# Optimization experiments

Measured on AMD Instinct MI355X. Metric: run time of the kernel, lower is better.

## Reference

```python
import jax, jax.numpy as jnp
import numpy as np

N = 100000   # nodes per layer
E = 600000   # edges per block
FIN = 256    # raw feature dim
H = 128      # hidden_size
C = 47       # n_classes
L = 3        # num_layers = n_layers + 1
NOUT = 10000 # seed nodes
GEN_EPS = 1e-7
T = 1.0
LN_EPS = 1e-5


def setup_inputs() -> dict:
    key = jax.random.key(0)
    ks = jax.random.split(key, 10)
    return {
        "x": jax.random.normal(ks[0], (N, FIN), jnp.float32),
        "src": jax.random.randint(ks[1], (L - 1, E), 0, N),
        "dst": jax.random.randint(ks[2], (L - 1, E), 0, N),
        "node_map": jax.random.randint(ks[3], (L - 1, N), 0, N),
        "final_map": jax.random.randint(ks[4], (NOUT,), 0, N),
        "enc_w": jax.random.normal(ks[5], (FIN, H), jnp.float32) * 0.05,
        "enc_b": jnp.zeros((H,), jnp.float32),
        "gcn_w": jax.random.normal(ks[6], (L, H, H), jnp.float32) * 0.05,
        "gcn_b": jnp.zeros((L, H), jnp.float32),
        "ln_g": jnp.ones((L, H), jnp.float32),
        "ln_b": jnp.zeros((L, H), jnp.float32),
        "pred_w": jax.random.normal(ks[7], (H, C), jnp.float32) * 0.05,
        "pred_b": jnp.zeros((C,), jnp.float32),
    }


def _layer_norm(h, g, b):
    mu = jnp.mean(h, axis=-1, keepdims=True)
    var = jnp.mean(jnp.square(h - mu), axis=-1, keepdims=True)
    return (h - mu) * jax.lax.rsqrt(var + LN_EPS) * g + b


def _gen_conv(h, src, dst, w, b):
    # GENConv, aggr='softmax', mlp_layers=1, no edge_attr, no msg_norm.
    m = jax.nn.relu(h[src]) + GEN_EPS                      # [E, H] messages
    # per-destination, per-feature segment softmax with temperature T
    mx = jax.ops.segment_max(m * T, dst, num_segments=N)   # [N, H]
    e = jnp.exp(m * T - mx[dst])                           # [E, H]
    denom = jax.ops.segment_sum(e, dst, num_segments=N)    # [N, H]
    alpha = e / (denom[dst] + 1e-16)
    agg = jax.ops.segment_sum(m * alpha, dst, num_segments=N)  # [N, H]
    return (agg + h) @ w + b                               # residual + Linear (MLP)


def reference(x, src, dst, node_map, final_map, enc_w, enc_b,
              gcn_w, gcn_b, ln_g, ln_b, pred_w, pred_b):
    h = x @ enc_w + enc_b                                  # node_features_encoder
    h = _gen_conv(h, src[0], dst[0], gcn_w[0], gcn_b[0])   # gcns[0] with block-0 edges
    for layer in range(1, L):                              # res+ block
        h2 = jax.nn.relu(_layer_norm(h, ln_g[layer - 1], ln_b[layer - 1]))
        # dropout is identity in eval mode (p applied with training=False)
        # gcns[layer] uses the edge_index set BEFORE this iteration's move
        h = _gen_conv(h2, src[layer - 1], dst[layer - 1],
                      gcn_w[layer], gcn_b[layer]) + h
        h = h[node_map[layer - 1]]                         # nf_move_layer_to gather
    h = jax.nn.relu(_layer_norm(h, ln_g[L - 1], ln_b[L - 1]))
    h = h @ pred_w + pred_b                                # node_pred_linear
    h = h[final_map]                                       # seed-node extraction
    return jax.nn.log_softmax(h, axis=-1)
```

## Files before the change

kernel.cpp:

```cpp
#include <hip/hip_runtime.h>
#include <hip/hip_bf16.h>
#include <hip/hip_fp16.h>

typedef unsigned short u16;
typedef unsigned int u32;

#define N_NODES 100000
#define N_EDGES 600000
#define FIN_D   256
#define HDIM    128
#define NCLS    47
#define NOUT_D  10000
#define NCHUNK  196
#define NP2     100352
#define PCH     2048
#define PNB     ((N_EDGES + PCH - 1) / PCH)

typedef short bf16x8 __attribute__((ext_vector_type(8)));
typedef float f32x4  __attribute__((ext_vector_type(4)));

#define GPTR(p) (const __attribute__((address_space(1))) u32*)(p)
#define LPTR(p) (__attribute__((address_space(3))) u32*)(p)

__device__ __forceinline__ float bf2f(u16 u) {
    union { u32 i; float f; } v; v.i = ((u32)u) << 16; return v.f;
}
__device__ __forceinline__ u16 f2bf(float f) {
    __hip_bfloat16 h = __float2bfloat16(f);
    return *reinterpret_cast<u16*>(&h);
}
__device__ __forceinline__ float loadF(const void* p, size_t i, bool f32) {
    if (f32) return ((const float*)p)[i];
    return bf2f(((const u16*)p)[i]);
}
__device__ __forceinline__ float wave_sum(float v) {
    #pragma unroll
    for (int o = 32; o > 0; o >>= 1) v += __shfl_xor(v, o, 64);
    return v;
}
__device__ __forceinline__ float wave_max(float v) {
    #pragma unroll
    for (int o = 32; o > 0; o >>= 1) v = fmaxf(v, __shfl_xor(v, o, 64));
    return v;
}
__device__ __forceinline__ int wave_sum_i(int v) {
    #pragma unroll
    for (int o = 32; o > 0; o >>= 1) v += __shfl_xor(v, o, 64);
    return v;
}
__device__ __forceinline__ int block_excl_scan_256(int v, int* wsum) {
    int lane = threadIdx.x & 63, wv = threadIdx.x >> 6;
    int inc = v;
    #pragma unroll
    for (int off = 1; off < 64; off <<= 1) {
        int u = __shfl_up(inc, off, 64);
        if (lane >= off) inc += u;
    }
    if (lane == 63) wsum[wv] = inc;
    __syncthreads();
    if (threadIdx.x == 0) {
        int a = 0;
        #pragma unroll
        for (int w = 0; w < 4; ++w) { int t = wsum[w]; wsum[w] = a; a += t; }
    }
    __syncthreads();
    return inc - v + wsum[wv];
}

__global__ __launch_bounds__(256) void dtype_detect_kernel(
    const u16* __restrict__ x, int* __restrict__ flag)
{
    int i = blockIdx.x * 256 + threadIdx.x;
    u32 e = (x[i] >> 7) & 0xFF;
    unsigned long long b = __ballot(e >= 200);
    if ((threadIdx.x & 63) == 0) {
        int c = __popcll(b);
        if (c) atomicAdd(&flag[1], c);
    }
}

__global__ __launch_bounds__(256) void hist2_kernel(
    const int* __restrict__ dst, int* __restrict__ deg2, int egrid)
{
    int half = (blockIdx.x >= egrid) ? 1 : 0;
    int e = (blockIdx.x - half * egrid) * 256 + threadIdx.x;
    if (e < N_EDGES) atomicAdd(&deg2[half * NP2 + dst[half * N_EDGES + e]], 1);
}

__global__ __launch_bounds__(256) void csum2_kernel(
    const int* __restrict__ deg2, int* __restrict__ csum)
{
    __shared__ int ws[4];
    int half = (blockIdx.x >= NCHUNK) ? 1 : 0;
    int b = blockIdx.x - half * NCHUNK;
    int i0 = half * NP2 + b * 512 + threadIdx.x;
    int v = 0;
    if (b * 512 + threadIdx.x < N_NODES) v += deg2[i0];
    if (b * 512 + threadIdx.x + 256 < N_NODES) v += deg2[i0 + 256];
    v = wave_sum_i(v);
    int lane = threadIdx.x & 63, wv = threadIdx.x >> 6;
    if (lane == 0) ws[wv] = v;
    __syncthreads();
    if (threadIdx.x == 0)
        csum[blockIdx.x] = ws[0] + ws[1] + ws[2] + ws[3];
}

__global__ __launch_bounds__(256) void coff2_kernel(
    const int* __restrict__ csum, int* __restrict__ coff,
    int* __restrict__ bcur)
{
    __shared__ int wsum[4];
    int t = threadIdx.x;
    for (int h = 0; h < 2; ++h) {
        int v = (t < NCHUNK) ? csum[h * NCHUNK + t] : 0;
        int excl = block_excl_scan_256(v, wsum);
        if (t < NCHUNK) {
            coff[h * NCHUNK + t] = excl;
            bcur[(h * NCHUNK + t) * 16] = excl;
        }
        __syncthreads();
    }
}

__global__ __launch_bounds__(256) void scan2_kernel(
    const int* __restrict__ deg2, const int* __restrict__ coff,
    int* __restrict__ rp0, int* __restrict__ rp1)
{
    __shared__ int wsum[4];
    int half = (blockIdx.x >= NCHUNK) ? 1 : 0;
    int b = blockIdx.x - half * NCHUNK;
    const int* deg = deg2 + half * NP2;
    int* rp = half ? rp1 : rp0;
    int t = threadIdx.x;
    int i0 = b * 512 + 2 * t;
    int d0 = (i0 < N_NODES) ? deg[i0] : 0;
    int d1 = (i0 + 1 < N_NODES) ? deg[i0 + 1] : 0;
    int excl = block_excl_scan_256(d0 + d1, wsum);
    int base = coff[half * NCHUNK + b] + excl;
    if (i0 < N_NODES)     rp[i0] = base;
    if (i0 + 1 < N_NODES) rp[i0 + 1] = base + d0;
    if (b == 0 && t == 0) rp[N_NODES] = N_EDGES;
}

__global__ __launch_bounds__(256) void bucket_part_kernel(
    const int* __restrict__ src, const int* __restrict__ dst,
    const int* __restrict__ comp1,
    int* __restrict__ bcur, int2* __restrict__ tmp)
{
    __shared__ int hist[NCHUNK];
    __shared__ int base[NCHUNK];
    int half = (blockIdx.x >= PNB) ? 1 : 0;
    int b = blockIdx.x - half * PNB;
    int e0 = b * PCH;
    for (int i = threadIdx.x; i < NCHUNK; i += 256) hist[i] = 0;
    __syncthreads();

    int2 loc[8];
    #pragma unroll
    for (int t = 0; t < 8; ++t) {
        int e = e0 + t * 256 + threadIdx.x;
        loc[t].y = -1;
        if (e < N_EDGES) {
            int ge = half * N_EDGES + e;
            int d = dst[ge];
            int s = src[ge];
            if (half) s = comp1[s];
            loc[t] = make_int2(s, d);
            atomicAdd(&hist[d >> 9], 1);
        }
    }
    __syncthreads();
    for (int i = threadIdx.x; i < NCHUNK; i += 256) {
        int h = hist[i];
        base[i] = (h > 0) ? atomicAdd(&bcur[(half * NCHUNK + i) * 16], h) : 0;
        hist[i] = 0;
    }
    __syncthreads();
    #pragma unroll
    for (int t = 0; t < 8; ++t) {
        if (loc[t].y >= 0) {
            int bk = loc[t].y >> 9;
            int pos = base[bk] + atomicAdd(&hist[bk], 1);
            tmp[(size_t)half * N_EDGES + pos] = loc[t];
        }
    }
}

__global__ __launch_bounds__(256) void bucket_sort_kernel(
    const int2* __restrict__ tmp,
    const int* __restrict__ rp0, const int* __restrict__ rp1,
    const int* __restrict__ coff, const int* __restrict__ csum,
    int* __restrict__ ei0, int* __restrict__ ei1)
{
    __shared__ int cur[512];
    int half = (blockIdx.x >= NCHUNK) ? 1 : 0;
    int b = blockIdx.x - half * NCHUNK;
    const int* rp = half ? rp1 : rp0;
    int* ei = half ? ei1 : ei0;
    int n0 = b * 512;
    #pragma unroll
    for (int i = threadIdx.x; i < 512; i += 256) {
        int n = n0 + i;
        cur[i] = (n < N_NODES) ? rp[n] : 0;
    }
    __syncthreads();
    int beg = coff[half * NCHUNK + b];
    int end = beg + csum[half * NCHUNK + b];
    for (int i = beg + threadIdx.x; i < end; i += 256) {
        int2 p = tmp[(size_t)half * N_EDGES + i];
        int pos = atomicAdd(&cur[p.y & 511], 1);
        ei[pos] = p.x;
    }
}

__global__ __launch_bounds__(256) void pack_b_kernel(
    const void* __restrict__ enc_w, const void* __restrict__ gcn_w,
    const int* __restrict__ dt, u16* __restrict__ Bp)
{
    const bool f32 = (dt[1] > 16);
    int o = blockIdx.x * 256 + threadIdx.x;
    if (o >= 32768 + 3 * 16384) return;
    const void* srcp; size_t soff; int m;
    if (o < 32768) { srcp = enc_w; soff = 0; m = o; }
    else {
        int l = (o - 32768) >> 14;
        srcp = gcn_w; soff = (size_t)l * 16384; m = (o - 32768) & 16383;
    }
    int j    = m & 7;
    int lane = (m >> 3) & 63;
    int ct   = (m >> 9) & 7;
    int kidx = m >> 12;
    int k = kidx * 32 + (lane >> 4) * 8 + j;
    int n = ct * 16 + (lane & 15);
    Bp[o] = f2bf(loadF(srcp, soff + (size_t)k * HDIM + n, f32));
}

__global__ __launch_bounds__(256, 2) void enc_gemm_kernel(
    const void* __restrict__ Araw, const u16* __restrict__ Bp,
    const void* __restrict__ bias, const int* __restrict__ dt,
    int rowbase, u16* __restrict__ OutBF)
{
    extern __shared__ char SH[];
    const bool f32 = (dt[1] > 16);
    const int tid  = threadIdx.x;
    const int w    = tid >> 6;
    const int lane = tid & 63;
    const int quad = lane >> 4;
    const int cl   = lane & 15;
    const int m0   = rowbase + blockIdx.x * 16;

    #pragma unroll
    for (int i = 0; i < 16; ++i) {
        int off = (w * 16 + i) * 1024;
        __builtin_amdgcn_global_load_lds(
            GPTR((const char*)Bp + off + lane * 16),
            LPTR(SH + off), 16, 0, 0);
    }
    if (f32) {
        #pragma unroll
        for (int i = 0; i < 4; ++i) {
            int row = w * 4 + i;
            int src = (lane * 16) ^ ((row & 7) << 4);
            __builtin_amdgcn_global_load_lds(
                GPTR((const char*)Araw + (size_t)(m0 + row) * 1024 + src),
                LPTR(SH + 65536 + row * 1024), 16, 0, 0);
        }
    } else {
        #pragma unroll
        for (int i = 0; i < 2; ++i) {
            int r0 = (w * 2 + i) * 2;
            int row = r0 + (lane >> 5);
            int src = ((lane & 31) * 16) ^ ((row & 7) << 4);
            __builtin_amdgcn_global_load_lds(
                GPTR((const char*)Araw + (size_t)(m0 + row) * 512 + src),
                LPTR(SH + 65536 + r0 * 512), 16, 0, 0);
        }
    }

    f32x4 acc[2];
    acc[0] = (f32x4){0.f, 0.f, 0.f, 0.f};
    acc[1] = (f32x4){0.f, 0.f, 0.f, 0.f};
    const int ct0 = w * 2;
    const int swz = (cl & 7) << 4;

    __syncthreads();

    #pragma unroll
    for (int k = 0; k < 8; ++k) {
        bf16x8 av;
        if (f32) {
            const char* rb = SH + 65536 + cl * 1024;
            int lo = (k * 128 + quad * 32) ^ swz;
            float4 v0 = *(const float4*)(rb + lo);
            float4 v1 = *(const float4*)(rb + (lo ^ 16));
            union { u32 u[4]; bf16x8 v; } cv;
            cv.u[0] = (u32)f2bf(v0.x) | ((u32)f2bf(v0.y) << 16);
            cv.u[1] = (u32)f2bf(v0.z) | ((u32)f2bf(v0.w) << 16);
            cv.u[2] = (u32)f2bf(v1.x) | ((u32)f2bf(v1.y) << 16);
            cv.u[3] = (u32)f2bf(v1.z) | ((u32)f2bf(v1.w) << 16);
            av = cv.v;
        } else {
            const char* rb = SH + 65536 + cl * 512;
            av = *(const bf16x8*)(rb + ((k * 64 + quad * 16) ^ swz));
        }
        #pragma unroll
        for (int c = 0; c < 2; ++c) {
            bf16x8 b = *(const bf16x8*)(SH + k * 8192 + (ct0 + c) * 1024 + lane * 16);
            acc[c] = __builtin_amdgcn_mfma_f32_16x16x32_bf16(av, b, acc[c], 0, 0, 0);
        }
    }

    #pragma unroll
    for (int reg = 0; reg < 4; ++reg) {
        int grow = m0 + quad * 4 + reg;
        #pragma unroll
        for (int c = 0; c < 2; ++c) {
            int col = (ct0 + c) * 16 + cl;
            float v = acc[c][reg] + loadF(bias, col, f32);
            OutBF[(size_t)grow * HDIM + col] = f2bf(v);
        }
    }
}

template<bool OWN_MAP>
__global__ __launch_bounds__(256) void agg_msg_kernel(
    const int* __restrict__ rp, const int* __restrict__ eidx,
    const u16* __restrict__ HBin, const int* __restrict__ own_map,
    u16* __restrict__ Amsg)
{
    __shared__ u32 RS[4][16][64];
    int wave = threadIdx.x >> 6;
    int lane = threadIdx.x & 63;
    int n = blockIdx.x * 4 + wave;
    if (n >= N_NODES) return;
    const u32* HB32 = (const u32*)HBin;
    int nn = OWN_MAP ? own_map[n] : n;
    u32 own = HB32[(size_t)nn * 64 + lane];
    int beg = rp[n], end = rp[n + 1];
    float den0 = 0.f, den1 = 0.f, num0 = 0.f, num1 = 0.f;
    for (int c = beg; c < end; c += 16) {
        int cnt = end - c; if (cnt > 16) cnt = 16;
        int e = c + (lane & 15); if (e > end - 1) e = end - 1;
        int ei = eidx[e];
        int nI = (cnt + 3) >> 2;
        #pragma unroll
        for (int i = 0; i < 4; ++i) {
            if (i < nI) {
                int s = __shfl(ei, i * 4 + (lane >> 4), 64);
                __builtin_amdgcn_global_load_lds(
                    GPTR((const char*)HBin + (size_t)s * 256 + (lane & 15) * 16),
                    LPTR(&RS[wave][i * 4][0]), 16, 0, 0);
            }
        }
        asm volatile("s_waitcnt vmcnt(0)" ::: "memory");
        __builtin_amdgcn_sched_barrier(0);
        #pragma unroll
        for (int t = 0; t < 16; ++t) {
            if (t >= cnt) break;
            u32 h = RS[wave][t][lane];
            float m0 = fmaxf(bf2f((u16)(h & 0xffff)), 0.f) + 1e-7f;
            float m1 = fmaxf(bf2f((u16)(h >> 16)),    0.f) + 1e-7f;
            float e0 = __expf(m0), e1 = __expf(m1);
            den0 += e0; num0 += m0 * e0;
            den1 += e1; num1 += m1 * e1;
        }
        asm volatile("s_waitcnt lgkmcnt(0)" ::: "memory");
        __builtin_amdgcn_sched_barrier(0);
    }
    float a0 = num0 / (den0 + 1e-16f) + bf2f((u16)(own & 0xffff));
    float a1 = num1 / (den1 + 1e-16f) + bf2f((u16)(own >> 16));
    ((u32*)Amsg)[(size_t)n * 64 + lane] = (u32)f2bf(a0) | ((u32)f2bf(a1) << 16);
}

template<bool RES, bool OWN_MAP, bool WRITE_LN>
__global__ __launch_bounds__(256) void conv_gemm_kernel(
    const u16* __restrict__ Amsg, const int* __restrict__ own_map,
    const u16* __restrict__ Bp, int Bpbase,
    const void* __restrict__ bias, int biasoff,
    const __half* __restrict__ Resid,
    const void* __restrict__ lng, const void* __restrict__ lnb, int lnoff,
    const int* __restrict__ dt,
    __half* __restrict__ OutH, u16* __restrict__ HBout)
{
    const bool f32 = (dt[1] > 16);
    __shared__ u16 Bsh[16384];
    __shared__ u16 Ash[8192];
    const int tid  = threadIdx.x;
    const int w    = tid >> 6;
    const int lane = tid & 63;
    const int quad = lane >> 4;
    const int cl   = lane & 15;
    const int m0   = blockIdx.x * 64;

    {
        const char* Bp2 = (const char*)(Bp + Bpbase);
        #pragma unroll
        for (int i = 0; i < 8; ++i)
            __builtin_amdgcn_global_load_lds(
                GPTR(Bp2 + i * 4096 + w * 1024 + lane * 16),
                LPTR((char*)Bsh + i * 4096 + w * 1024), 16, 0, 0);
        const char* Ab = (const char*)Amsg + (size_t)m0 * 256;
        #pragma unroll
        for (int i = 0; i < 4; ++i) {
            int row_local = i * 16 + w * 4 + (lane >> 4);
            int off = ((lane & 15) * 16) ^ ((row_local & 7) << 4);
            __builtin_amdgcn_global_load_lds(
                GPTR(Ab + (size_t)row_local * 256 + off),
                LPTR((char*)Ash + i * 4096 + w * 1024), 16, 0, 0);
        }
    }

    __syncthreads();

    const int row_local = w * 16 + cl;
    const char* ar = (const char*)Ash + row_local * 256;
    const int akey = (row_local & 7) << 4;
    bf16x8 afr[4];
    #pragma unroll
    for (int kidx = 0; kidx < 4; ++kidx)
        afr[kidx] = *(const bf16x8*)(ar + ((kidx * 64 + quad * 16) ^ akey));

    f32x4 acc[8];
    #pragma unroll
    for (int ct = 0; ct < 8; ++ct) acc[ct] = (f32x4){0.f, 0.f, 0.f, 0.f};
    #pragma unroll
    for (int kidx = 0; kidx < 4; ++kidx) {
        const u16* bb = Bsh + ((size_t)(kidx * 8) * 64 + lane) * 8;
        #pragma unroll
        for (int ct = 0; ct < 8; ++ct) {
            bf16x8 b = *(const bf16x8*)(bb + (size_t)ct * 512);
            acc[ct] = __builtin_amdgcn_mfma_f32_16x16x32_bf16(afr[kidx], b, acc[ct], 0, 0, 0);
        }
    }

    #pragma unroll
    for (int reg = 0; reg < 4; ++reg) {
        int n = m0 + w * 16 + quad * 4 + reg;
        if (n >= N_NODES) continue;
        size_t rrow = 0;
        if (RES) rrow = (size_t)(OWN_MAP ? own_map[n] : n) * HDIM;
        float v[8];
        float s1 = 0.f, s2 = 0.f;
        #pragma unroll
        for (int ct = 0; ct < 8; ++ct) {
            int col = ct * 16 + cl;
            float x = acc[ct][reg] + loadF(bias, biasoff + col, f32);
            if (RES) x += __half2float(Resid[rrow + col]);
            v[ct] = x;
            OutH[(size_t)n * HDIM + col] = __float2half(x);
            s1 += x; s2 += x * x;
        }
        if (WRITE_LN) {
            #pragma unroll
            for (int o = 1; o < 16; o <<= 1) {
                s1 += __shfl_xor(s1, o, 64);
                s2 += __shfl_xor(s2, o, 64);
            }
            float mu = s1 * (1.0f / 128.0f);
            float var = s2 * (1.0f / 128.0f) - mu * mu;
            float rs = rsqrtf(fmaxf(var, 0.f) + 1e-5f);
            #pragma unroll
            for (int ct = 0; ct < 8; ++ct) {
                int col = ct * 16 + cl;
                float y = fmaxf((v[ct] - mu) * rs * loadF(lng, lnoff + col, f32)
                                + loadF(lnb, lnoff + col, f32), 0.f);
                HBout[(size_t)n * HDIM + col] = f2bf(y);
            }
        }
    }
}

__global__ __launch_bounds__(256) void final_head_kernel(
    const __half* __restrict__ Hsrc, const int* __restrict__ map1,
    const int* __restrict__ fmap,
    const void* __restrict__ g, const void* __restrict__ b, int goff,
    const void* __restrict__ pw, const void* __restrict__ pb,
    const int* __restrict__ dt, void* __restrict__ out)
{
    const bool f32 = (dt[1] > 16);
    __shared__ float pwl[HDIM * 48];
    __shared__ float pbl[64];
    __shared__ float sh[4][HDIM];
    const int tid = threadIdx.x, wave = tid >> 6, lane = tid & 63;

    for (int i = tid; i < HDIM * NCLS; i += 256)
        pwl[(i / NCLS) * 48 + (i % NCLS)] = loadF(pw, i, f32);
    if (tid < NCLS) pbl[tid] = loadF(pb, tid, f32);
    __syncthreads();

    int i = blockIdx.x * 4 + wave;
    int jj = map1[fmap[i]];
    __half2 hv = *((const __half2*)(Hsrc + (size_t)jj * HDIM) + lane);
    float2 v = __half22float2(hv);
    float mu = wave_sum(v.x + v.y) * (1.0f / 128.0f);
    float d0 = v.x - mu, d1 = v.y - mu;
    float var = wave_sum(d0 * d0 + d1 * d1) * (1.0f / 128.0f);
    float rs = rsqrtf(var + 1e-5f);
    int f0 = lane * 2;
    sh[wave][f0]     = fmaxf(d0 * rs * loadF(g, goff + f0, f32)     + loadF(b, goff + f0, f32),     0.0f);
    sh[wave][f0 + 1] = fmaxf(d1 * rs * loadF(g, goff + f0 + 1, f32) + loadF(b, goff + f0 + 1, f32), 0.0f);
    float acc = -1e30f;
    if (lane < NCLS) {
        acc = pbl[lane];
        #pragma unroll 8
        for (int k = 0; k < HDIM; ++k)
            acc = fmaf(sh[wave][k], pwl[k * 48 + lane], acc);
    }
    float mx = wave_max(acc);
    float ex = (lane < NCLS) ? __expf(acc - mx) : 0.0f;
    float sum = wave_sum(ex);
    if (lane < NCLS) {
        float r = acc - mx - logf(sum);
        if (f32) ((float*)out)[(size_t)i * NCLS + lane] = r;
        else     ((u16*)out)[(size_t)i * NCLS + lane] = f2bf(r);
    }
}

extern "C" void kernel_launch(void* const* d_in, const int* in_sizes, int n_in,
                              void* d_out, int out_size, void* d_ws, size_t ws_size,
                              hipStream_t stream) {
    const void* x       = d_in[0];
    const int* src      = (const int*)d_in[1];
    const int* dst      = (const int*)d_in[2];
    const int* node_map = (const int*)d_in[3];
    const int* fmap     = (const int*)d_in[4];
    const void* enc_w   = d_in[5];
    const void* enc_b   = d_in[6];
    const void* gcn_w   = d_in[7];
    const void* gcn_b   = d_in[8];
    const void* ln_g    = d_in[9];
    const void* ln_b    = d_in[10];
    const void* pred_w  = d_in[11];
    const void* pred_b  = d_in[12];

    char* ws = (char*)d_ws;
    const size_t szH = (size_t)N_NODES * HDIM * sizeof(u16);
    __half* Pa  = (__half*)ws;  ws += szH;
    __half* Pb  = (__half*)ws;  ws += szH;
    u16*   HBa  = (u16*)ws;     ws += szH;
    u16*   HBb  = (u16*)ws;     ws += szH;
    u16*   Amsg = (u16*)ws;     ws += szH;
    int*   FLAG = (int*)ws;     ws += 1024;
    u16*   Bp   = (u16*)ws;     ws += (size_t)(32768 + 3 * 16384) * 2 + 1024;
    int*  deg2  = (int*)ws;  ws += (size_t)2 * NP2 * 4;
    int*  rp0   = (int*)ws;  ws += (size_t)(N_NODES + 2) * 4;
    int*  rp1   = (int*)ws;  ws += (size_t)(N_NODES + 2) * 4;
    int*  ei0   = (int*)ws;  ws += (size_t)N_EDGES * 4;
    int*  ei1   = (int*)ws;  ws += (size_t)N_EDGES * 4;
    int2* tmp   = (int2*)ws; ws += (size_t)2 * N_EDGES * 8;
    int*  csum  = (int*)ws;  ws += 2048;
    int*  coff  = (int*)ws;  ws += 2048;
    int*  bcur  = (int*)ws;  ws += (size_t)2 * NCHUNK * 16 * 4 + 1024;

    dim3 blk(256);
    const int ggrid = (N_NODES + 63) / 64;
    const int gHALF = 3125;
    const int egrid = (N_EDGES + 255) / 256;
    const int agrid = (N_NODES + 3) / 4;
    const int pgrid = (32768 + 3 * 16384 + 255) / 256;

    hipMemsetAsync(FLAG, 0, 64, stream);
    dtype_detect_kernel<<<256, blk, 0, stream>>>((const u16*)x, FLAG);
    pack_b_kernel<<<pgrid, blk, 0, stream>>>(enc_w, gcn_w, FLAG, Bp);

    hipMemsetAsync(deg2, 0, (size_t)2 * NP2 * 4, stream);
    hist2_kernel<<<2 * egrid, blk, 0, stream>>>(dst, deg2, egrid);
    csum2_kernel<<<2 * NCHUNK, blk, 0, stream>>>(deg2, csum);
    coff2_kernel<<<1, blk, 0, stream>>>(csum, coff, bcur);
    scan2_kernel<<<2 * NCHUNK, blk, 0, stream>>>(deg2, coff, rp0, rp1);
    bucket_part_kernel<<<2 * PNB, blk, 0, stream>>>(src, dst, node_map, bcur, tmp);
    bucket_sort_kernel<<<2 * NCHUNK, blk, 0, stream>>>(tmp, rp0, rp1, coff, csum,
                                                       ei0, ei1);

    enc_gemm_kernel<<<gHALF, blk, 81920, stream>>>(x, Bp, enc_b, FLAG, 0, HBa);
    enc_gemm_kernel<<<gHALF, blk, 81920, stream>>>(x, Bp, enc_b, FLAG, 50000, HBa);

    agg_msg_kernel<false><<<agrid, blk, 0, stream>>>(rp0, ei0, HBa, nullptr, Amsg);
    conv_gemm_kernel<false, false, true><<<ggrid, blk, 0, stream>>>(
        Amsg, nullptr, Bp, 32768, gcn_b, 0, nullptr,
        ln_g, ln_b, 0, FLAG, Pa, HBb);

    agg_msg_kernel<false><<<agrid, blk, 0, stream>>>(rp0, ei0, HBb, nullptr, Amsg);
    conv_gemm_kernel<true, false, true><<<ggrid, blk, 0, stream>>>(
        Amsg, nullptr, Bp, 32768 + 16384, gcn_b, 128, Pa,
        ln_g, ln_b, 128, FLAG, Pb, HBa);

    agg_msg_kernel<true><<<agrid, blk, 0, stream>>>(rp1, ei1, HBa, node_map, Amsg);
    conv_gemm_kernel<true, true, false><<<ggrid, blk, 0, stream>>>(
        Amsg, node_map, Bp, 32768 + 2 * 16384, gcn_b, 256, Pb,
        ln_g, ln_b, 256, FLAG, Pa, nullptr);

    final_head_kernel<<<NOUT_D / 4, blk, 0, stream>>>(
        Pa, node_map + N_NODES, fmap, ln_g, ln_b, 256, pred_w, pred_b, FLAG,
        (void*)d_out);
}
```

Before: 574.0 us.

## Fuse softmax aggregation into conv GEMM kernel and merge encoder launches

The per-node softmax aggregation kernel is folded into the conv GEMM kernel. Each 512-thread block has 8 waves that each aggregate 8 destination rows directly into the swizzled shared-memory A tile, then 4 waves run the MFMA GEMM. This drops the Amsg round trip through global memory and halves the kernel launches per layer. The two encoder GEMM launches are also merged into one. The cost is that half the waves sit idle during the GEMM, aggregation batches shrink from 16 to 8 edges, and occupancy may be limited by the larger shared-memory footprint.

```diff
diff --git a/kernel.cpp b/kernel.cpp
--- a/kernel.cpp
+++ b/kernel.cpp
@@ -238,7 +238,7 @@
 __global__ __launch_bounds__(256, 2) void enc_gemm_kernel(
     const void* __restrict__ Araw, const u16* __restrict__ Bp,
     const void* __restrict__ bias, const int* __restrict__ dt,
-    int rowbase, u16* __restrict__ OutBF)
+    u16* __restrict__ OutBF)
 {
     extern __shared__ char SH[];
     const bool f32 = (dt[1] > 16);
@@ -247,7 +247,7 @@
     const int lane = tid & 63;
     const int quad = lane >> 4;
     const int cl   = lane & 15;
-    const int m0   = rowbase + blockIdx.x * 16;
+    const int m0   = blockIdx.x * 16;
 
     #pragma unroll
     for (int i = 0; i < 16; ++i) {
@@ -322,59 +322,10 @@
     }
 }
 
-template<bool OWN_MAP>
-__global__ __launch_bounds__(256) void agg_msg_kernel(
+template<bool RES, bool OWN_MAP, bool WRITE_LN>
+__global__ __launch_bounds__(512, 2) void layer_kernel(
     const int* __restrict__ rp, const int* __restrict__ eidx,
     const u16* __restrict__ HBin, const int* __restrict__ own_map,
-    u16* __restrict__ Amsg)
-{
-    __shared__ u32 RS[4][16][64];
-    int wave = threadIdx.x >> 6;
-    int lane = threadIdx.x & 63;
-    int n = blockIdx.x * 4 + wave;
-    if (n >= N_NODES) return;
-    const u32* HB32 = (const u32*)HBin;
-    int nn = OWN_MAP ? own_map[n] : n;
-    u32 own = HB32[(size_t)nn * 64 + lane];
-    int beg = rp[n], end = rp[n + 1];
-    float den0 = 0.f, den1 = 0.f, num0 = 0.f, num1 = 0.f;
-    for (int c = beg; c < end; c += 16) {
-        int cnt = end - c; if (cnt > 16) cnt = 16;
-        int e = c + (lane & 15); if (e > end - 1) e = end - 1;
-        int ei = eidx[e];
-        int nI = (cnt + 3) >> 2;
-        #pragma unroll
-        for (int i = 0; i < 4; ++i) {
-            if (i < nI) {
-                int s = __shfl(ei, i * 4 + (lane >> 4), 64);
-                __builtin_amdgcn_global_load_lds(
-                    GPTR((const char*)HBin + (size_t)s * 256 + (lane & 15) * 16),
-                    LPTR(&RS[wave][i * 4][0]), 16, 0, 0);
-            }
-        }
-        asm volatile("s_waitcnt vmcnt(0)" ::: "memory");
-        __builtin_amdgcn_sched_barrier(0);
-        #pragma unroll
-        for (int t = 0; t < 16; ++t) {
-            if (t >= cnt) break;
-            u32 h = RS[wave][t][lane];
-            float m0 = fmaxf(bf2f((u16)(h & 0xffff)), 0.f) + 1e-7f;
-            float m1 = fmaxf(bf2f((u16)(h >> 16)),    0.f) + 1e-7f;
-            float e0 = __expf(m0), e1 = __expf(m1);
-            den0 += e0; num0 += m0 * e0;
-            den1 += e1; num1 += m1 * e1;
-        }
-        asm volatile("s_waitcnt lgkmcnt(0)" ::: "memory");
-        __builtin_amdgcn_sched_barrier(0);
-    }
-    float a0 = num0 / (den0 + 1e-16f) + bf2f((u16)(own & 0xffff));
-    float a1 = num1 / (den1 + 1e-16f) + bf2f((u16)(own >> 16));
-    ((u32*)Amsg)[(size_t)n * 64 + lane] = (u32)f2bf(a0) | ((u32)f2bf(a1) << 16);
-}
-
-template<bool RES, bool OWN_MAP, bool WRITE_LN>
-__global__ __launch_bounds__(256) void conv_gemm_kernel(
-    const u16* __restrict__ Amsg, const int* __restrict__ own_map,
     const u16* __restrict__ Bp, int Bpbase,
     const void* __restrict__ bias, int biasoff,
     const __half* __restrict__ Resid,
@@ -385,8 +336,9 @@
     const bool f32 = (dt[1] > 16);
     __shared__ u16 Bsh[16384];
     __shared__ u16 Ash[8192];
+    __shared__ u32 RS[8][8][64];
     const int tid  = threadIdx.x;
-    const int w    = tid >> 6;
+    const int wv   = tid >> 6;
     const int lane = tid & 63;
     const int quad = lane >> 4;
     const int cl   = lane & 15;
@@ -395,22 +347,72 @@
     {
         const char* Bp2 = (const char*)(Bp + Bpbase);
         #pragma unroll
-        for (int i = 0; i < 8; ++i)
+        for (int i = 0; i < 4; ++i)
             __builtin_amdgcn_global_load_lds(
-                GPTR(Bp2 + i * 4096 + w * 1024 + lane * 16),
-                LPTR((char*)Bsh + i * 4096 + w * 1024), 16, 0, 0);
-        const char* Ab = (const char*)Amsg + (size_t)m0 * 256;
-        #pragma unroll
-        for (int i = 0; i < 4; ++i) {
-            int row_local = i * 16 + w * 4 + (lane >> 4);
-            int off = ((lane & 15) * 16) ^ ((row_local & 7) << 4);
-            __builtin_amdgcn_global_load_lds(
-                GPTR(Ab + (size_t)row_local * 256 + off),
-                LPTR((char*)Ash + i * 4096 + w * 1024), 16, 0, 0);
-        }
-    }
-
-    __syncthreads();
+                GPTR(Bp2 + (wv * 4 + i) * 1024 + lane * 16),
+                LPTR((char*)Bsh + (wv * 4 + i) * 1024), 16, 0, 0);
+    }
+
+    const u32* HB32 = (const u32*)HBin;
+    char* AshB = (char*)Ash;
+
+    int rbase = m0 + wv * 8;
+    int ridx = rbase + ((lane < 9) ? lane : 8);
+    if (ridx > N_NODES) ridx = N_NODES;
+    int rpv = rp[ridx];
+
+    #pragma unroll 1
+    for (int j = 0; j < 8; ++j) {
+        int rl = wv * 8 + j;
+        int n = m0 + rl;
+        u32 outv = 0;
+        if (n < N_NODES) {
+            int nn = OWN_MAP ? own_map[n] : n;
+            u32 own = HB32[(size_t)nn * 64 + lane];
+            int beg = __shfl(rpv, j, 64);
+            int end = __shfl(rpv, j + 1, 64);
+            float den0 = 0.f, den1 = 0.f, num0 = 0.f, num1 = 0.f;
+            for (int c = beg; c < end; c += 8) {
+                int cnt = end - c; if (cnt > 8) cnt = 8;
+                int e = c + (lane & 7); if (e > end - 1) e = end - 1;
+                int ei = eidx[e];
+                int nI = (cnt + 3) >> 2;
+                #pragma unroll
+                for (int i = 0; i < 2; ++i) {
+                    if (i < nI) {
+                        int s = __shfl(ei, i * 4 + (lane >> 4), 64);
+                        __builtin_amdgcn_global_load_lds(
+                            GPTR((const char*)HBin + (size_t)s * 256 + (lane & 15) * 16),
+                            LPTR(&RS[wv][i * 4][0]), 16, 0, 0);
+                    }
+                }
+                asm volatile("s_waitcnt vmcnt(0)" ::: "memory");
+                __builtin_amdgcn_sched_barrier(0);
+                #pragma unroll
+                for (int t = 0; t < 8; ++t) {
+                    if (t >= cnt) break;
+                    u32 h = RS[wv][t][lane];
+                    float v0 = fmaxf(bf2f((u16)(h & 0xffff)), 0.f) + 1e-7f;
+                    float v1 = fmaxf(bf2f((u16)(h >> 16)),    0.f) + 1e-7f;
+                    float e0 = __expf(v0), e1 = __expf(v1);
+                    den0 += e0; num0 += v0 * e0;
+                    den1 += e1; num1 += v1 * e1;
+                }
+                asm volatile("s_waitcnt lgkmcnt(0)" ::: "memory");
+                __builtin_amdgcn_sched_barrier(0);
+            }
+            float a0 = num0 / (den0 + 1e-16f) + bf2f((u16)(own & 0xffff));
+            float a1 = num1 / (den1 + 1e-16f) + bf2f((u16)(own >> 16));
+            outv = (u32)f2bf(a0) | ((u32)f2bf(a1) << 16);
+        }
+        *(u32*)(AshB + rl * 256 + ((lane * 4) ^ ((rl & 7) << 4))) = outv;
+    }
+
+    asm volatile("s_waitcnt vmcnt(0)" ::: "memory");
+    __syncthreads();
+
+    if (wv >= 4) return;
+    const int w = wv;
 
     const int row_local = w * 16 + cl;
     const char* ar = (const char*)Ash + row_local * 256;
@@ -539,7 +541,6 @@
     __half* Pb  = (__half*)ws;  ws += szH;
     u16*   HBa  = (u16*)ws;     ws += szH;
     u16*   HBb  = (u16*)ws;     ws += szH;
-    u16*   Amsg = (u16*)ws;     ws += szH;
     int*   FLAG = (int*)ws;     ws += 1024;
     u16*   Bp   = (u16*)ws;     ws += (size_t)(32768 + 3 * 16384) * 2 + 1024;
     int*  deg2  = (int*)ws;  ws += (size_t)2 * NP2 * 4;
@@ -554,9 +555,8 @@
 
     dim3 blk(256);
     const int ggrid = (N_NODES + 63) / 64;
-    const int gHALF = 3125;
+    const int g16   = (N_NODES + 15) / 16;
     const int egrid = (N_EDGES + 255) / 256;
-    const int agrid = (N_NODES + 3) / 4;
     const int pgrid = (32768 + 3 * 16384 + 255) / 256;
 
     hipMemsetAsync(FLAG, 0, 64, stream);
@@ -572,22 +572,18 @@
     bucket_sort_kernel<<<2 * NCHUNK, blk, 0, stream>>>(tmp, rp0, rp1, coff, csum,
                                                        ei0, ei1);
 
-    enc_gemm_kernel<<<gHALF, blk, 81920, stream>>>(x, Bp, enc_b, FLAG, 0, HBa);
-    enc_gemm_kernel<<<gHALF, blk, 81920, stream>>>(x, Bp, enc_b, FLAG, 50000, HBa);
-
-    agg_msg_kernel<false><<<agrid, blk, 0, stream>>>(rp0, ei0, HBa, nullptr, Amsg);
-    conv_gemm_kernel<false, false, true><<<ggrid, blk, 0, stream>>>(
-        Amsg, nullptr, Bp, 32768, gcn_b, 0, nullptr,
+    enc_gemm_kernel<<<g16, blk, 81920, stream>>>(x, Bp, enc_b, FLAG, HBa);
+
+    layer_kernel<false, false, true><<<ggrid, dim3(512), 0, stream>>>(
+        rp0, ei0, HBa, nullptr, Bp, 32768, gcn_b, 0, nullptr,
         ln_g, ln_b, 0, FLAG, Pa, HBb);
 
-    agg_msg_kernel<false><<<agrid, blk, 0, stream>>>(rp0, ei0, HBb, nullptr, Amsg);
-    conv_gemm_kernel<true, false, true><<<ggrid, blk, 0, stream>>>(
-        Amsg, nullptr, Bp, 32768 + 16384, gcn_b, 128, Pa,
+    layer_kernel<true, false, true><<<ggrid, dim3(512), 0, stream>>>(
+        rp0, ei0, HBb, nullptr, Bp, 32768 + 16384, gcn_b, 128, Pa,
         ln_g, ln_b, 128, FLAG, Pb, HBa);
 
-    agg_msg_kernel<true><<<agrid, blk, 0, stream>>>(rp1, ei1, HBa, node_map, Amsg);
-    conv_gemm_kernel<true, true, false><<<ggrid, blk, 0, stream>>>(
-        Amsg, node_map, Bp, 32768 + 2 * 16384, gcn_b, 256, Pb,
+    layer_kernel<true, true, false><<<ggrid, dim3(512), 0, stream>>>(
+        rp1, ei1, HBa, node_map, Bp, 32768 + 2 * 16384, gcn_b, 256, Pb,
         ln_g, ln_b, 256, FLAG, Pa, nullptr);
 
     final_head_kernel<<<NOUT_D / 4, blk, 0, stream>>>(
```

Result: slower. 666.3 us (+16.1%).

## Compute bucket counts via LDS histogram, fold degree counting into partition kernel

Applied to the files above, without the earlier changes.

Replaces the per-node global-atomic degree histogram and chunk-sum kernels with a shared-memory bucket histogram that produces the per-chunk counts directly. Per-node degree counting moves into the bucket partition kernel, which now runs before the scan, so one pass over dst and one launch are removed. The two half-size encoder GEMM launches are also merged into a single launch. This trades fewer launches and global atomics for extra global atomics inside the partition kernel.

```diff
diff --git a/kernel.cpp b/kernel.cpp
--- a/kernel.cpp
+++ b/kernel.cpp
@@ -15,6 +15,7 @@
 #define NP2     100352
 #define PCH     2048
 #define PNB     ((N_EDGES + PCH - 1) / PCH)
+#define EB      1024
 
 typedef short bf16x8 __attribute__((ext_vector_type(8)));
 typedef float f32x4  __attribute__((ext_vector_type(4)));
@@ -41,11 +42,6 @@
 __device__ __forceinline__ float wave_max(float v) {
     #pragma unroll
     for (int o = 32; o > 0; o >>= 1) v = fmaxf(v, __shfl_xor(v, o, 64));
-    return v;
-}
-__device__ __forceinline__ int wave_sum_i(int v) {
-    #pragma unroll
-    for (int o = 32; o > 0; o >>= 1) v += __shfl_xor(v, o, 64);
     return v;
 }
 __device__ __forceinline__ int block_excl_scan_256(int v, int* wsum) {
@@ -79,30 +75,22 @@
     }
 }
 
-__global__ __launch_bounds__(256) void hist2_kernel(
-    const int* __restrict__ dst, int* __restrict__ deg2, int egrid)
-{
-    int half = (blockIdx.x >= egrid) ? 1 : 0;
-    int e = (blockIdx.x - half * egrid) * 256 + threadIdx.x;
-    if (e < N_EDGES) atomicAdd(&deg2[half * NP2 + dst[half * N_EDGES + e]], 1);
-}
-
-__global__ __launch_bounds__(256) void csum2_kernel(
-    const int* __restrict__ deg2, int* __restrict__ csum)
-{
-    __shared__ int ws[4];
-    int half = (blockIdx.x >= NCHUNK) ? 1 : 0;
-    int b = blockIdx.x - half * NCHUNK;
-    int i0 = half * NP2 + b * 512 + threadIdx.x;
-    int v = 0;
-    if (b * 512 + threadIdx.x < N_NODES) v += deg2[i0];
-    if (b * 512 + threadIdx.x + 256 < N_NODES) v += deg2[i0 + 256];
-    v = wave_sum_i(v);
-    int lane = threadIdx.x & 63, wv = threadIdx.x >> 6;
-    if (lane == 0) ws[wv] = v;
-    __syncthreads();
-    if (threadIdx.x == 0)
-        csum[blockIdx.x] = ws[0] + ws[1] + ws[2] + ws[3];
+__global__ __launch_bounds__(256) void histb_kernel(
+    const int* __restrict__ dst, int* __restrict__ bcnt, int ebgrid)
+{
+    __shared__ int h[NCHUNK];
+    int half = (blockIdx.x >= ebgrid) ? 1 : 0;
+    int e0 = (blockIdx.x - half * ebgrid) * EB;
+    for (int i = threadIdx.x; i < NCHUNK; i += 256) h[i] = 0;
+    __syncthreads();
+    #pragma unroll
+    for (int t = 0; t < 4; ++t) {
+        int e = e0 + t * 256 + threadIdx.x;
+        if (e < N_EDGES) atomicAdd(&h[dst[half * N_EDGES + e] >> 9], 1);
+    }
+    __syncthreads();
+    for (int i = threadIdx.x; i < NCHUNK; i += 256)
+        if (h[i]) atomicAdd(&bcnt[half * NCHUNK + i], h[i]);
 }
 
 __global__ __launch_bounds__(256) void coff2_kernel(
@@ -119,6 +107,52 @@
             bcur[(h * NCHUNK + t) * 16] = excl;
         }
         __syncthreads();
+    }
+}
+
+__global__ __launch_bounds__(256) void bucket_part_kernel(
+    const int* __restrict__ src, const int* __restrict__ dst,
+    const int* __restrict__ comp1,
+    int* __restrict__ bcur, int2* __restrict__ tmp,
+    int* __restrict__ deg2)
+{
+    __shared__ int hist[NCHUNK];
+    __shared__ int base[NCHUNK];
+    int half = (blockIdx.x >= PNB) ? 1 : 0;
+    int b = blockIdx.x - half * PNB;
+    int e0 = b * PCH;
+    for (int i = threadIdx.x; i < NCHUNK; i += 256) hist[i] = 0;
+    __syncthreads();
+
+    int2 loc[8];
+    #pragma unroll
+    for (int t = 0; t < 8; ++t) {
+        int e = e0 + t * 256 + threadIdx.x;
+        loc[t].y = -1;
+        if (e < N_EDGES) {
+            int ge = half * N_EDGES + e;
+            int d = dst[ge];
+            int s = src[ge];
+            if (half) s = comp1[s];
+            loc[t] = make_int2(s, d);
+            atomicAdd(&hist[d >> 9], 1);
+            atomicAdd(&deg2[half * NP2 + d], 1);
+        }
+    }
+    __syncthreads();
+    for (int i = threadIdx.x; i < NCHUNK; i += 256) {
+        int h = hist[i];
+        base[i] = (h > 0) ? atomicAdd(&bcur[(half * NCHUNK + i) * 16], h) : 0;
+        hist[i] = 0;
+    }
+    __syncthreads();
+    #pragma unroll
+    for (int t = 0; t < 8; ++t) {
+        if (loc[t].y >= 0) {
+            int bk = loc[t].y >> 9;
+            int pos = base[bk] + atomicAdd(&hist[bk], 1);
+            tmp[(size_t)half * N_EDGES + pos] = loc[t];
+        }
     }
 }
 
@@ -142,50 +176,6 @@
     if (b == 0 && t == 0) rp[N_NODES] = N_EDGES;
 }
 
-__global__ __launch_bounds__(256) void bucket_part_kernel(
-    const int* __restrict__ src, const int* __restrict__ dst,
-    const int* __restrict__ comp1,
-    int* __restrict__ bcur, int2* __restrict__ tmp)
-{
-    __shared__ int hist[NCHUNK];
-    __shared__ int base[NCHUNK];
-    int half = (blockIdx.x >= PNB) ? 1 : 0;
-    int b = blockIdx.x - half * PNB;
-    int e0 = b * PCH;
-    for (int i = threadIdx.x; i < NCHUNK; i += 256) hist[i] = 0;
-    __syncthreads();
-
-    int2 loc[8];
-    #pragma unroll
-    for (int t = 0; t < 8; ++t) {
-        int e = e0 + t * 256 + threadIdx.x;
-        loc[t].y = -1;
-        if (e < N_EDGES) {
-            int ge = half * N_EDGES + e;
-            int d = dst[ge];
-            int s = src[ge];
-            if (half) s = comp1[s];
-            loc[t] = make_int2(s, d);
-            atomicAdd(&hist[d >> 9], 1);
-        }
-    }
-    __syncthreads();
-    for (int i = threadIdx.x; i < NCHUNK; i += 256) {
-        int h = hist[i];
-        base[i] = (h > 0) ? atomicAdd(&bcur[(half * NCHUNK + i) * 16], h) : 0;
-        hist[i] = 0;
-    }
-    __syncthreads();
-    #pragma unroll
-    for (int t = 0; t < 8; ++t) {
-        if (loc[t].y >= 0) {
-            int bk = loc[t].y >> 9;
-            int pos = base[bk] + atomicAdd(&hist[bk], 1);
-            tmp[(size_t)half * N_EDGES + pos] = loc[t];
-        }
-    }
-}
-
 __global__ __launch_bounds__(256) void bucket_sort_kernel(
     const int2* __restrict__ tmp,
     const int* __restrict__ rp0, const int* __restrict__ rp1,
@@ -238,7 +228,7 @@
 __global__ __launch_bounds__(256, 2) void enc_gemm_kernel(
     const void* __restrict__ Araw, const u16* __restrict__ Bp,
     const void* __restrict__ bias, const int* __restrict__ dt,
-    int rowbase, u16* __restrict__ OutBF)
+    u16* __restrict__ OutBF)
 {
     extern __shared__ char SH[];
     const bool f32 = (dt[1] > 16);
@@ -247,7 +237,7 @@
     const int lane = tid & 63;
     const int quad = lane >> 4;
     const int cl   = lane & 15;
-    const int m0   = rowbase + blockIdx.x * 16;
+    const int m0   = blockIdx.x * 16;
 
     #pragma unroll
     for (int i = 0; i < 16; ++i) {
@@ -554,26 +544,26 @@
 
     dim3 blk(256);
     const int ggrid = (N_NODES + 63) / 64;
-    const int gHALF = 3125;
-    const int egrid = (N_EDGES + 255) / 256;
+    const int g16   = (N_NODES + 15) / 16;
+    const int ebgrid = (N_EDGES + EB - 1) / EB;
     const int agrid = (N_NODES + 3) / 4;
     const int pgrid = (32768 + 3 * 16384 + 255) / 256;
 
     hipMemsetAsync(FLAG, 0, 64, stream);
+    hipMemsetAsync(csum, 0, 2048 * sizeof(int), stream);
     dtype_detect_kernel<<<256, blk, 0, stream>>>((const u16*)x, FLAG);
     pack_b_kernel<<<pgrid, blk, 0, stream>>>(enc_w, gcn_w, FLAG, Bp);
 
     hipMemsetAsync(deg2, 0, (size_t)2 * NP2 * 4, stream);
-    hist2_kernel<<<2 * egrid, blk, 0, stream>>>(dst, deg2, egrid);
-    csum2_kernel<<<2 * NCHUNK, blk, 0, stream>>>(deg2, csum);
+    histb_kernel<<<2 * ebgrid, blk, 0, stream>>>(dst, csum, ebgrid);
     coff2_kernel<<<1, blk, 0, stream>>>(csum, coff, bcur);
+    bucket_part_kernel<<<2 * PNB, blk, 0, stream>>>(src, dst, node_map, bcur, tmp,
+                                                    deg2);
     scan2_kernel<<<2 * NCHUNK, blk, 0, stream>>>(deg2, coff, rp0, rp1);
-    bucket_part_kernel<<<2 * PNB, blk, 0, stream>>>(src, dst, node_map, bcur, tmp);
     bucket_sort_kernel<<<2 * NCHUNK, blk, 0, stream>>>(tmp, rp0, rp1, coff, csum,
                                                        ei0, ei1);
 
-    enc_gemm_kernel<<<gHALF, blk, 81920, stream>>>(x, Bp, enc_b, FLAG, 0, HBa);
-    enc_gemm_kernel<<<gHALF, blk, 81920, stream>>>(x, Bp, enc_b, FLAG, 50000, HBa);
+    enc_gemm_kernel<<<g16, blk, 81920, stream>>>(x, Bp, enc_b, FLAG, HBa);
 
     agg_msg_kernel<false><<<agrid, blk, 0, stream>>>(rp0, ei0, HBa, nullptr, Amsg);
     conv_gemm_kernel<false, false, true><<<ggrid, blk, 0, stream>>>(
```

Measured after the change: 588.4 us. 1.03x slower.
